# Optimization experiments

Measured on AMD Instinct MI355X. Metric: run time of the kernel, lower is better.

## Reference

```python
import jax, jax.numpy as jnp
import numpy as np

N, E, D, C, H1 = 50000, 800000, 128, 8, 2


def setup_inputs() -> dict:
    key = jax.random.key(0)
    ks = jax.random.split(key, 14)
    s = lambda k, sh: (jax.random.normal(k, sh, jnp.float32) * 0.05)
    return {
        "x": jax.random.normal(ks[0], (N, D), jnp.float32),
        "edge_index": jax.random.randint(ks[1], (2, E), 0, N, dtype=jnp.int32),
        # conv1: GATConv(D, D, heads=2, concat=True)
        "W1": s(ks[2], (D, H1 * D)),
        "att1_src": s(ks[3], (H1, D)),
        "att1_dst": s(ks[4], (H1, D)),
        "b1": s(ks[5], (H1 * D,)),
        # conv2: GATConv(2D, D, heads=1, concat=False)
        "W2": s(ks[6], (H1 * D, D)),
        "att2_src": s(ks[7], (1, D)),
        "att2_dst": s(ks[8], (1, D)),
        "b2": s(ks[9], (D,)),
        # MLP head
        "Wm1": s(ks[10], (D, D)),
        "bm1": s(ks[11], (D,)),
        "Wm2": s(ks[12], (D, C)),
        "bm2": s(ks[13], (C,)),
    }


def gat_conv(x, src, dst, W, a_src, a_dst, b, heads, out_ch, concat):
    """PyG GATConv (eval mode): self-loops added by caller, softmax over
    edges grouped by destination node, negative_slope=0.2."""
    n = x.shape[0]
    h = (x @ W).reshape(n, heads, out_ch)              # [N,H,F]
    alpha_src = jnp.einsum('nhf,hf->nh', h, a_src)     # [N,H]
    alpha_dst = jnp.einsum('nhf,hf->nh', h, a_dst)     # [N,H]
    e = jax.nn.leaky_relu(alpha_src[src] + alpha_dst[dst], 0.2)  # [E,H]
    e_max = jax.ops.segment_max(e, dst, num_segments=n)
    ex = jnp.exp(e - e_max[dst])
    denom = jax.ops.segment_sum(ex, dst, num_segments=n)
    alpha = ex / jnp.maximum(denom[dst], 1e-16)        # [E,H]
    out = jax.ops.segment_sum(h[src] * alpha[:, :, None], dst, num_segments=n)
    out = out.reshape(n, heads * out_ch) if concat else out.mean(axis=1)
    return out + b


def reference(x, edge_index, W1, att1_src, att1_dst, b1,
              W2, att2_src, att2_dst, b2, Wm1, bm1, Wm2, bm2):
    n = x.shape[0]
    loop = jnp.arange(n, dtype=edge_index.dtype)
    src = jnp.concatenate([edge_index[0], loop])  # add_self_loops=True
    dst = jnp.concatenate([edge_index[1], loop])
    h = jax.nn.elu(gat_conv(x, src, dst, W1, att1_src, att1_dst, b1, H1, D, True))
    h = jax.nn.elu(gat_conv(h, src, dst, W2, att2_src, att2_dst, b2, 1, D, False))
    h = jax.nn.relu(h @ Wm1 + bm1)
    return jax.nn.relu(h @ Wm2 + bm2)
```

## Files before the change

kernel.cpp:

```cpp
#include <hip/hip_runtime.h>
#include <hip/hip_bf16.h>


__device__ __forceinline__ float lrelu(float x){ return x > 0.f ? x : 0.2f*x; }
__device__ __forceinline__ float elu_f(float x){ return x > 0.f ? x : __expf(x) - 1.f; }
__device__ __forceinline__ unsigned short f2bf(float f){
  __hip_bfloat16 h = __float2bfloat16(f);
  return *reinterpret_cast<unsigned short*>(&h);
}
__device__ __forceinline__ float bflo(unsigned int u){ return __uint_as_float(u << 16); }
__device__ __forceinline__ float bfhi(unsigned int u){ return __uint_as_float(u & 0xffff0000u); }
__device__ __forceinline__ unsigned int packbf(float a, float b){
  return (unsigned int)f2bf(a) | ((unsigned int)f2bf(b) << 16);
}

typedef __attribute__((ext_vector_type(8))) short bf16x8;
typedef __attribute__((ext_vector_type(4))) float f32x4;

__global__ void prep_kernel(const float* __restrict__ W1, unsigned short* __restrict__ BT1a,
                            unsigned short* __restrict__ BT1b,
                            const float* __restrict__ W2, unsigned short* __restrict__ BT2,
                            const float* __restrict__ Wm1, unsigned short* __restrict__ BT3,
                            const float* __restrict__ a1s, const float* __restrict__ a1d,
                            float* __restrict__ va, int* __restrict__ bcount,
                            int* __restrict__ gcur, int NB){
  int idx = blockIdx.x*256 + threadIdx.x;
  const int S1 = 128*256, S2 = 128*256, S3 = 128*128;
  if (idx < S1){
    int k = idx >> 8, c = idx & 255;
    unsigned short v = f2bf(W1[idx]);
    if (c < 128) BT1a[c*128 + k] = v;
    else         BT1b[(c-128)*128 + k] = v;
  } else if (idx < S1 + S2){
    int j = idx - S1;
    int k = j >> 7, n = j & 127;
    BT2[n*256 + k] = f2bf(W2[j]);
  } else if (idx < S1 + S2 + S3){
    int j = idx - S1 - S2;
    int k = j >> 7, n = j & 127;
    BT3[n*128 + k] = f2bf(Wm1[j]);
  } else if (idx < S1 + S2 + S3 + 512){
    int j = idx - S1 - S2 - S3;
    int v = j >> 7, k = j & 127;
    const float* avec = (v < 2) ? a1s : a1d;
    int head = v & 1;
    const float4* wrow = (const float4*)(W1 + (size_t)k*256 + head*128);
    const float4* arow = (const float4*)(avec + head*128);
    float s = 0.f;
    #pragma unroll 8
    for (int f = 0; f < 32; ++f){
      float4 w = wrow[f], a = arow[f];
      s += w.x*a.x + w.y*a.y + w.z*a.z + w.w*a.w;
    }
    va[j] = s;
  } else if (idx < S1 + S2 + S3 + 512 + 2048){
    int z = idx - (S1 + S2 + S3 + 512);
    if (z < 1024){ if (z < NB) bcount[z] = 0; }
    else { z -= 1024; if (z < NB) gcur[z] = 0; }
  }
}

__global__ __launch_bounds__(256) void f2bf_hist_kernel(
    const float* __restrict__ x, unsigned short* __restrict__ xb, int N,
    const float* __restrict__ va, float* __restrict__ as1, float* __restrict__ ad1,
    const int* __restrict__ dst, int E, int* __restrict__ bcount, int NB, int nbConv)
{
  __shared__ int h[1024];
  if ((int)blockIdx.x < nbConv){
    int i = blockIdx.x*256 + threadIdx.x;
    int total = N*32;
    float4 v = make_float4(0.f,0.f,0.f,0.f);
    if (i < total){
      v = ((const float4*)x)[i];
      ushort4 u; u.x=f2bf(v.x); u.y=f2bf(v.y); u.z=f2bf(v.z); u.w=f2bf(v.w);
      ((ushort4*)xb)[i] = u;
    }
    int c = (i & 31) << 2;
    float4 vs0 = *(const float4*)(va + c);
    float4 vs1 = *(const float4*)(va + 128 + c);
    float4 vd0 = *(const float4*)(va + 256 + c);
    float4 vd1 = *(const float4*)(va + 384 + c);
    float s0 = v.x*vs0.x + v.y*vs0.y + v.z*vs0.z + v.w*vs0.w;
    float s1 = v.x*vs1.x + v.y*vs1.y + v.z*vs1.z + v.w*vs1.w;
    float d0 = v.x*vd0.x + v.y*vd0.y + v.z*vd0.z + v.w*vd0.w;
    float d1 = v.x*vd1.x + v.y*vd1.y + v.z*vd1.z + v.w*vd1.w;
    #pragma unroll
    for (int m = 1; m <= 16; m <<= 1){
      s0 += __shfl_xor(s0, m); s1 += __shfl_xor(s1, m);
      d0 += __shfl_xor(d0, m); d1 += __shfl_xor(d1, m);
    }
    if ((i & 31) == 0 && i < total){
      int n = i >> 5;
      *(float2*)(as1 + 2*n) = make_float2(s0, s1);
      *(float2*)(ad1 + 2*n) = make_float2(d0, d1);
    }
  } else {
    for (int i = threadIdx.x; i < NB; i += 256) h[i] = 0;
    __syncthreads();
    int b0 = blockIdx.x - nbConv;
    for (int e = b0*256 + threadIdx.x; e < E; e += 64*256)
      atomicAdd(&h[dst[e] >> 6], 1);
    __syncthreads();
    for (int i = threadIdx.x; i < NB; i += 256)
      if (h[i]) atomicAdd(&bcount[i], h[i]);
  }
}

__global__ __launch_bounds__(256) void bscatter_kernel(
    const int* __restrict__ src, const int* __restrict__ dst, int E,
    const int* __restrict__ bcount, int* __restrict__ boff,
    int* __restrict__ gcur, unsigned int* __restrict__ pairs, int NB)
{
  __shared__ int h[1024];
  __shared__ int runbase[1024];
  __shared__ int sc[1024];
  const int t = threadIdx.x;
  const int e0 = blockIdx.x * 4096;

  for (int i = t; i < 1024; i += 256) sc[i] = (i < NB) ? bcount[i] : 0;
  for (int i = t; i < NB; i += 256) h[i] = 0;
  __syncthreads();
  for (int d = 1; d < 1024; d <<= 1){
    int v0 = (t       >= d) ? sc[t       - d] : 0;
    int v1 = (t + 256 >= d) ? sc[t + 256 - d] : 0;
    int v2 = (t + 512 >= d) ? sc[t + 512 - d] : 0;
    int v3 = (t + 768 >= d) ? sc[t + 768 - d] : 0;
    __syncthreads();
    sc[t] += v0; sc[t+256] += v1; sc[t+512] += v2; sc[t+768] += v3;
    __syncthreads();
  }
  if (blockIdx.x == 0){
    for (int i = t; i <= NB; i += 256) boff[i] = i ? sc[i-1] : 0;
  }

  int myb[16]; unsigned int myw[16];
  #pragma unroll
  for (int q = 0; q < 16; ++q){
    int e = e0 + q*256 + t;
    int b = -1; unsigned int w = 0;
    if (e < E){
      int d = dst[e];
      b = d >> 6;
      w = ((unsigned int)(d & 63) << 26) | (unsigned int)src[e];
      atomicAdd(&h[b], 1);
    }
    myb[q] = b; myw[q] = w;
  }
  __syncthreads();
  for (int i = t; i < NB; i += 256)
    runbase[i] = h[i] ? atomicAdd(&gcur[i], h[i]) : 0;
  __syncthreads();
  for (int i = t; i < NB; i += 256) h[i] = 0;
  __syncthreads();
  #pragma unroll
  for (int q = 0; q < 16; ++q){
    if (myb[q] >= 0){
      int off = atomicAdd(&h[myb[q]], 1);
      int base = myb[q] ? sc[myb[q]-1] : 0;
      pairs[(size_t)base + runbase[myb[q]] + off] = myw[q];
    }
  }
}

__global__ __launch_bounds__(256) void bbuild_kernel(
    const unsigned int* __restrict__ pairs, const int* __restrict__ boff,
    int* __restrict__ rowptr, int* __restrict__ csr, int N)
{
  __shared__ int deg[64], offs[64], cur[64];
  const int b = blockIdx.x;
  const int t = threadIdx.x;
  const int n0 = b << 6;
  const int nNodes = min(64, N - n0);
  const int p0 = boff[b], p1 = boff[b+1];
  const int base = p0 + n0;
  if (t < 64) deg[t] = (t < nNodes) ? 1 : 0;
  __syncthreads();
  for (int i = p0 + t; i < p1; i += 256)
    atomicAdd(&deg[pairs[i] >> 26], 1);
  __syncthreads();
  if (t < 64){
    int x = deg[t];
    #pragma unroll
    for (int d = 1; d < 64; d <<= 1){
      int y = __shfl_up(x, d);
      if (t >= d) x += y;
    }
    offs[t] = x - deg[t];
    cur[t] = 1;
    if (t < nNodes){
      rowptr[n0 + t + 1] = base + x;
      csr[base + x - deg[t]] = n0 + t;
    }
    if (b == 0 && t == 0) rowptr[0] = 0;
  }
  __syncthreads();
  for (int i = p0 + t; i < p1; i += 256){
    unsigned int w = pairs[i];
    int dl = w >> 26;
    int s  = (int)(w & 0x03ffffffu);
    int off = atomicAdd(&cur[dl], 1);
    csr[base + offs[dl] + off] = s;
  }
}

__device__ __forceinline__ void gemm_core(
    const unsigned short* __restrict__ A, int lda,
    const unsigned short* __restrict__ BT, int M, int K, int r0,
    unsigned short* a_s, unsigned short* b_s, f32x4 (&acc)[4][4])
{
  const int tid  = threadIdx.x;
  const int lane = tid & 63, wv = tid >> 6;
  const int mh = (wv & 1)*64, nh = (wv >> 1)*64;
  const int l15 = lane & 15, quad = lane >> 4;
  const int srow = tid >> 3, skc = tid & 7;

  #pragma unroll
  for (int i = 0; i < 4; ++i)
    #pragma unroll
    for (int j = 0; j < 4; ++j)
      #pragma unroll
      for (int r = 0; r < 4; ++r) acc[i][j][r] = 0.f;

  for (int k0 = 0; k0 < K; k0 += 64){
    #pragma unroll
    for (int it = 0; it < 4; ++it){
      int row = it*32 + srow;
      int grow = r0 + row;
      uint4 v = make_uint4(0u,0u,0u,0u);
      if (grow < M) v = *(const uint4*)(A + (size_t)grow*lda + k0 + skc*8);
      *(uint4*)(&a_s[row*72 + skc*8]) = v;
    }
    #pragma unroll
    for (int it = 0; it < 4; ++it){
      int row = it*32 + srow;
      uint4 v = *(const uint4*)(BT + (size_t)row*K + k0 + skc*8);
      *(uint4*)(&b_s[row*72 + skc*8]) = v;
    }
    __syncthreads();
    #pragma unroll
    for (int ks = 0; ks < 64; ks += 32){
      bf16x8 af[4], bfr[4];
      #pragma unroll
      for (int i = 0; i < 4; ++i)
        af[i] = *(const bf16x8*)(&a_s[(mh + i*16 + l15)*72 + ks + quad*8]);
      #pragma unroll
      for (int j = 0; j < 4; ++j)
        bfr[j] = *(const bf16x8*)(&b_s[(nh + j*16 + l15)*72 + ks + quad*8]);
      #pragma unroll
      for (int i = 0; i < 4; ++i)
        #pragma unroll
        for (int j = 0; j < 4; ++j)
          acc[i][j] = __builtin_amdgcn_mfma_f32_16x16x32_bf16(bfr[j], af[i], acc[i][j], 0, 0, 0);
    }
    __syncthreads();
  }
}

__global__ __launch_bounds__(256) void gemm_conv1_kernel(
    const unsigned short* __restrict__ xa, const unsigned short* __restrict__ BT1a,
    const unsigned short* __restrict__ BT1b, unsigned short* __restrict__ out1b,
    int M, const float* __restrict__ b1)
{
  __shared__ unsigned short a_s[128*72];
  __shared__ unsigned short b_s[128*72];
  const int hx = blockIdx.x;
  const unsigned short* A  = xa + hx*128;
  const unsigned short* BT = hx ? BT1b : BT1a;
  unsigned short* C = out1b + hx*128;
  const float* bias = b1 + hx*128;
  const int r0 = blockIdx.y*128;
  f32x4 acc[4][4];
  gemm_core(A, 256, BT, M, 128, r0, a_s, b_s, acc);

  const int lane = threadIdx.x & 63, wv = threadIdx.x >> 6;
  const int mh = (wv & 1)*64, nh = (wv >> 1)*64;
  const int l15 = lane & 15, quad = lane >> 4;
  #pragma unroll
  for (int i = 0; i < 4; ++i){
    int m = r0 + mh + i*16 + l15;
    if (m < M){
      #pragma unroll
      for (int j = 0; j < 4; ++j){
        int n = nh + j*16 + quad*4;
        float4 bb = *(const float4*)(bias + n);
        ushort4 u;
        u.x = f2bf(elu_f(acc[i][j][0] + bb.x));
        u.y = f2bf(elu_f(acc[i][j][1] + bb.y));
        u.z = f2bf(elu_f(acc[i][j][2] + bb.z));
        u.w = f2bf(elu_f(acc[i][j][3] + bb.w));
        *(ushort4*)(C + (size_t)m*256 + n) = u;
      }
    }
  }
}

__global__ __launch_bounds__(256) void gemm_conv2_kernel(
    const unsigned short* __restrict__ out1b, const unsigned short* __restrict__ BT2,
    unsigned short* __restrict__ h2b, int M,
    const float* __restrict__ a2s, const float* __restrict__ a2d,
    float* __restrict__ as2, float* __restrict__ ad2)
{
  __shared__ unsigned short a_s[128*72];
  __shared__ unsigned short b_s[128*72];
  __shared__ float part_s[128][2];
  __shared__ float part_d[128][2];
  const int r0 = blockIdx.y*128;
  f32x4 acc[4][4];
  gemm_core(out1b, 256, BT2, M, 256, r0, a_s, b_s, acc);

  const int tid = threadIdx.x;
  const int lane = tid & 63, wv = tid >> 6;
  const int mh = (wv & 1)*64, nh = (wv >> 1)*64;
  const int l15 = lane & 15, quad = lane >> 4;
  #pragma unroll
  for (int i = 0; i < 4; ++i){
    int m = r0 + mh + i*16 + l15;
    float ps = 0.f, pd = 0.f;
    #pragma unroll
    for (int j = 0; j < 4; ++j){
      int n = nh + j*16 + quad*4;
      float4 wsv = *(const float4*)(a2s + n);
      float4 wdv = *(const float4*)(a2d + n);
      float v0 = acc[i][j][0], v1 = acc[i][j][1], v2 = acc[i][j][2], v3 = acc[i][j][3];
      ps += v0*wsv.x + v1*wsv.y + v2*wsv.z + v3*wsv.w;
      pd += v0*wdv.x + v1*wdv.y + v2*wdv.z + v3*wdv.w;
      if (m < M){
        ushort4 u;
        u.x = f2bf(v0); u.y = f2bf(v1); u.z = f2bf(v2); u.w = f2bf(v3);
        *(ushort4*)(h2b + (size_t)m*128 + n) = u;
      }
    }
    ps += __shfl_xor(ps, 16); ps += __shfl_xor(ps, 32);
    pd += __shfl_xor(pd, 16); pd += __shfl_xor(pd, 32);
    if (quad == 0){
      part_s[mh + i*16 + l15][wv >> 1] = ps;
      part_d[mh + i*16 + l15][wv >> 1] = pd;
    }
  }
  __syncthreads();
  if (tid < 128){
    int gm = r0 + tid;
    if (gm < M){
      as2[gm] = part_s[tid][0] + part_s[tid][1];
      ad2[gm] = part_d[tid][0] + part_d[tid][1];
    }
  }
}

__global__ __launch_bounds__(256) void gemm_mlp_kernel(
    const unsigned short* __restrict__ gb, const unsigned short* __restrict__ BT3,
    int M, const float* __restrict__ bm1, const float* __restrict__ Wm2,
    const float* __restrict__ bm2, float* __restrict__ out)
{
  __shared__ unsigned short a_s[128*72];
  __shared__ unsigned short b_s[128*72];
  __shared__ float wm2_s[128*8];
  __shared__ float part[128][2][8];
  const int tid = threadIdx.x;
  {
    int i4 = tid*4;
    *(float4*)(&wm2_s[i4]) = *(const float4*)(Wm2 + i4);
  }
  const int r0 = blockIdx.y*128;
  f32x4 acc[4][4];
  gemm_core(gb, 128, BT3, M, 128, r0, a_s, b_s, acc);

  const int lane = tid & 63, wv = tid >> 6;
  const int mh = (wv & 1)*64, nh = (wv >> 1)*64;
  const int l15 = lane & 15, quad = lane >> 4;
  #pragma unroll
  for (int i = 0; i < 4; ++i){
    float po[8];
    #pragma unroll
    for (int o = 0; o < 8; ++o) po[o] = 0.f;
    #pragma unroll
    for (int j = 0; j < 4; ++j){
      int n = nh + j*16 + quad*4;
      float4 bb = *(const float4*)(bm1 + n);
      #pragma unroll
      for (int r = 0; r < 4; ++r){
        float hcol = fmaxf(acc[i][j][r] + ((const float*)&bb)[r], 0.f);
        const float* wr = &wm2_s[(n + r)*8];
        #pragma unroll
        for (int o = 0; o < 8; ++o) po[o] += hcol*wr[o];
      }
    }
    #pragma unroll
    for (int o = 0; o < 8; ++o){
      po[o] += __shfl_xor(po[o], 16);
      po[o] += __shfl_xor(po[o], 32);
    }
    if (quad == 0){
      #pragma unroll
      for (int o = 0; o < 8; ++o) part[mh + i*16 + l15][wv >> 1][o] = po[o];
    }
  }
  __syncthreads();
  if (tid < 128){
    int gm = r0 + tid;
    if (gm < M){
      float4 o0, o1;
      o0.x = fmaxf(part[tid][0][0] + part[tid][1][0] + bm2[0], 0.f);
      o0.y = fmaxf(part[tid][0][1] + part[tid][1][1] + bm2[1], 0.f);
      o0.z = fmaxf(part[tid][0][2] + part[tid][1][2] + bm2[2], 0.f);
      o0.w = fmaxf(part[tid][0][3] + part[tid][1][3] + bm2[3], 0.f);
      o1.x = fmaxf(part[tid][0][4] + part[tid][1][4] + bm2[4], 0.f);
      o1.y = fmaxf(part[tid][0][5] + part[tid][1][5] + bm2[5], 0.f);
      o1.z = fmaxf(part[tid][0][6] + part[tid][1][6] + bm2[6], 0.f);
      o1.w = fmaxf(part[tid][0][7] + part[tid][1][7] + bm2[7], 0.f);
      *(float4*)(out + (size_t)gm*8)     = o0;
      *(float4*)(out + (size_t)gm*8 + 4) = o1;
    }
  }
}

#define AGG1_FMA(u, a0v, a1v) do{ \
    float f0 = bflo(u.x), f1 = bfhi(u.x), f2v = bflo(u.y), f3 = bfhi(u.y); \
    float f4 = bflo(u.z), f5 = bfhi(u.z), f6 = bflo(u.w), f7 = bfhi(u.w); \
    acc0[0] += a0v*f0; acc0[1] += a0v*f1; acc0[2] += a0v*f2v; acc0[3] += a0v*f3; \
    acc0[4] += a0v*f4; acc0[5] += a0v*f5; acc0[6] += a0v*f6;  acc0[7] += a0v*f7; \
    acc1[0] += a1v*f0; acc1[1] += a1v*f1; acc1[2] += a1v*f2v; acc1[3] += a1v*f3; \
    acc1[4] += a1v*f4; acc1[5] += a1v*f5; acc1[6] += a1v*f6;  acc1[7] += a1v*f7; \
  }while(0)

#define AGG2_FMA(u, av) do{ \
    acc[0] += av*bflo(u.x); acc[1] += av*bfhi(u.x); \
    acc[2] += av*bflo(u.y); acc[3] += av*bfhi(u.y); \
    acc[4] += av*bflo(u.z); acc[5] += av*bfhi(u.z); \
    acc[6] += av*bflo(u.w); acc[7] += av*bfhi(u.w); \
  }while(0)

__global__ __launch_bounds__(256) void agg1x_kernel(
    const unsigned short* __restrict__ xb, const float* __restrict__ as_,
    const float* __restrict__ ad_, const int* __restrict__ rowptr, const int* __restrict__ csr,
    unsigned short* __restrict__ xa, int N)
{
  const int wv = threadIdx.x >> 6, lane = threadIdx.x & 63;
  const int ql = lane & 15;
  const int n = blockIdx.x*16 + wv*4 + (lane >> 4);
  const bool valid = n < N;
  int start = 0, end = 0;
  float2 adv = make_float2(0.f, 0.f);
  if (valid){ start = rowptr[n]; end = rowptr[n+1]; adv = *(const float2*)(ad_ + 2*n); }

  int jl = start + ql;
  bool have = valid && (jl < end);
  int s_l = 0;
  float p0 = 0.f, p1 = 0.f;
  if (have){
    s_l = csr[jl];
    float2 av = *(const float2*)(as_ + 2*s_l);
    p0 = __expf(lrelu(av.x + adv.x));
    p1 = __expf(lrelu(av.y + adv.y));
  }
  float l0 = p0, l1 = p1;
  for (int j = jl + 16; j < end; j += 16){
    int s = csr[j];
    float2 av = *(const float2*)(as_ + 2*s);
    l0 += __expf(lrelu(av.x + adv.x));
    l1 += __expf(lrelu(av.y + adv.y));
  }
  #pragma unroll
  for (int msk = 1; msk <= 8; msk <<= 1){
    l0 += __shfl_xor(l0, msk);
    l1 += __shfl_xor(l1, msk);
  }
  float inv0 = 1.f / fmaxf(l0, 1e-16f);
  float inv1 = 1.f / fmaxf(l1, 1e-16f);
  float a0_l = p0 * inv0;
  float a1_l = p1 * inv1;

  float acc0[8], acc1[8];
  #pragma unroll
  for (int i = 0; i < 8; ++i){ acc0[i] = 0.f; acc1[i] = 0.f; }
  const int c = ql << 3;
  const unsigned short* hp = xb + c;

  #pragma unroll
  for (int half = 0; half < 2; ++half){
    uint4 u[8]; float b0[8], b1[8];
    #pragma unroll
    for (int t = 0; t < 8; ++t){
      int tt = half*8 + t;
      int sA = __shfl(s_l, tt, 16);
      b0[t] = __shfl(a0_l, tt, 16);
      b1[t] = __shfl(a1_l, tt, 16);
      u[t] = *(const uint4*)(hp + (sA << 7));
    }
    #pragma unroll
    for (int t = 0; t < 8; ++t) AGG1_FMA(u[t], b0[t], b1[t]);
  }
  for (int jb = start + 16; jb < end; jb += 16){
    int jl2 = jb + ql;
    int s2 = 0; float a0_2 = 0.f, a1_2 = 0.f;
    if (jl2 < end){
      s2 = csr[jl2];
      float2 av = *(const float2*)(as_ + 2*s2);
      a0_2 = __expf(lrelu(av.x + adv.x)) * inv0;
      a1_2 = __expf(lrelu(av.y + adv.y)) * inv1;
    }
    int cnt2 = min(16, end - jb);
    for (int t2 = 0; t2 < cnt2; t2 += 2){
      int   sA  = __shfl(s2, t2, 16),   sB  = __shfl(s2, t2+1, 16);
      float a0A = __shfl(a0_2, t2, 16), a0B = __shfl(a0_2, t2+1, 16);
      float a1A = __shfl(a1_2, t2, 16), a1B = __shfl(a1_2, t2+1, 16);
      uint4 uA = *(const uint4*)(hp + (sA << 7));
      uint4 uB = *(const uint4*)(hp + (sB << 7));
      AGG1_FMA(uA, a0A, a1A);
      AGG1_FMA(uB, a0B, a1B);
    }
  }

  if (valid){
    uint4 u0, u1;
    u0.x = packbf(acc0[0], acc0[1]); u0.y = packbf(acc0[2], acc0[3]);
    u0.z = packbf(acc0[4], acc0[5]); u0.w = packbf(acc0[6], acc0[7]);
    u1.x = packbf(acc1[0], acc1[1]); u1.y = packbf(acc1[2], acc1[3]);
    u1.z = packbf(acc1[4], acc1[5]); u1.w = packbf(acc1[6], acc1[7]);
    *(uint4*)(xa + (size_t)n*256 + c)       = u0;
    *(uint4*)(xa + (size_t)n*256 + 128 + c) = u1;
  }
}

__global__ __launch_bounds__(256) void agg2_kernel(
    const unsigned short* __restrict__ h2b, const float* __restrict__ as_,
    const float* __restrict__ ad_, const int* __restrict__ rowptr, const int* __restrict__ csr,
    const float* __restrict__ b2, unsigned short* __restrict__ outb, int N)
{
  const int wv = threadIdx.x >> 6, lane = threadIdx.x & 63;
  const int ql = lane & 15;
  const int n = blockIdx.x*16 + wv*4 + (lane >> 4);
  const bool valid = n < N;
  int start = 0, end = 0;
  float adn = 0.f;
  if (valid){ start = rowptr[n]; end = rowptr[n+1]; adn = ad_[n]; }

  int jl = start + ql;
  bool have = valid && (jl < end);
  int s_l = 0;
  float p_l = 0.f;
  if (have){
    s_l = csr[jl];
    p_l = __expf(lrelu(as_[s_l] + adn));
  }
  float l = p_l;
  for (int j = jl + 16; j < end; j += 16)
    l += __expf(lrelu(as_[csr[j]] + adn));
  #pragma unroll
  for (int msk = 1; msk <= 8; msk <<= 1) l += __shfl_xor(l, msk);
  float inv = 1.f / fmaxf(l, 1e-16f);
  float a_l = p_l * inv;

  float acc[8];
  #pragma unroll
  for (int i = 0; i < 8; ++i) acc[i] = 0.f;
  const int c = ql << 3;
  const unsigned short* hp = h2b + c;

  #pragma unroll
  for (int half = 0; half < 2; ++half){
    uint4 u[8]; float av[8];
    #pragma unroll
    for (int t = 0; t < 8; ++t){
      int tt = half*8 + t;
      int sA = __shfl(s_l, tt, 16);
      av[t] = __shfl(a_l, tt, 16);
      u[t] = *(const uint4*)(hp + (sA << 7));
    }
    #pragma unroll
    for (int t = 0; t < 8; ++t) AGG2_FMA(u[t], av[t]);
  }
  for (int jb = start + 16; jb < end; jb += 16){
    int jl2 = jb + ql;
    int s2 = 0; float a2 = 0.f;
    if (jl2 < end){
      s2 = csr[jl2];
      a2 = __expf(lrelu(as_[s2] + adn)) * inv;
    }
    int cnt2 = min(16, end - jb);
    for (int t2 = 0; t2 < cnt2; t2 += 2){
      int   sA = __shfl(s2, t2, 16),  sB = __shfl(s2, t2+1, 16);
      float aA = __shfl(a2, t2, 16),  aB = __shfl(a2, t2+1, 16);
      uint4 uA = *(const uint4*)(hp + (sA << 7));
      uint4 uB = *(const uint4*)(hp + (sB << 7));
      AGG2_FMA(uA, aA);
      AGG2_FMA(uB, aB);
    }
  }

  if (valid){
    float4 bb0 = *(const float4*)(b2 + c);
    float4 bb1 = *(const float4*)(b2 + c + 4);
    float o[8];
    o[0]=elu_f(acc[0]+bb0.x); o[1]=elu_f(acc[1]+bb0.y);
    o[2]=elu_f(acc[2]+bb0.z); o[3]=elu_f(acc[3]+bb0.w);
    o[4]=elu_f(acc[4]+bb1.x); o[5]=elu_f(acc[5]+bb1.y);
    o[6]=elu_f(acc[6]+bb1.z); o[7]=elu_f(acc[7]+bb1.w);
    uint4 up;
    up.x = packbf(o[0], o[1]); up.y = packbf(o[2], o[3]);
    up.z = packbf(o[4], o[5]); up.w = packbf(o[6], o[7]);
    *(uint4*)(outb + (size_t)n*128 + c) = up;
  }
}

extern "C" void kernel_launch(void* const* d_in, const int* in_sizes, int n_in,
                              void* d_out, int out_size, void* d_ws, size_t ws_size,
                              hipStream_t stream)
{
  (void)n_in; (void)out_size; (void)ws_size;
  const float* x   = (const float*)d_in[0];
  const int*   ei  = (const int*)d_in[1];
  const float* W1  = (const float*)d_in[2];
  const float* a1s = (const float*)d_in[3];
  const float* a1d = (const float*)d_in[4];
  const float* b1  = (const float*)d_in[5];
  const float* W2  = (const float*)d_in[6];
  const float* a2s = (const float*)d_in[7];
  const float* a2d = (const float*)d_in[8];
  const float* b2  = (const float*)d_in[9];
  const float* Wm1 = (const float*)d_in[10];
  const float* bm1 = (const float*)d_in[11];
  const float* Wm2 = (const float*)d_in[12];
  const float* bm2 = (const float*)d_in[13];
  float* out = (float*)d_out;

  const int N = in_sizes[0] / 128;
  const int E = in_sizes[1] / 2;
  const int NB = (N + 63) >> 6;
  const int* srcp = ei;
  const int* dstp = ei + E;

  char* ws = (char*)d_ws;
  unsigned short* xb    = (unsigned short*)ws;
  unsigned short* xa    = (unsigned short*)(ws + (size_t)N*256);
  unsigned short* out1b = (unsigned short*)(ws + (size_t)N*768);
  unsigned short* h2b   = (unsigned short*)(ws + (size_t)N*1280);
  char* tail = ws + (size_t)N*1536;
  unsigned short* BT1a = (unsigned short*)tail;
  unsigned short* BT1b = BT1a + 128*128;
  unsigned short* BT2  = BT1b + 128*128;
  unsigned short* BT3  = BT2 + 128*256;
  float* va   = (float*)(BT3 + 128*128);
  float* as1  = va + 512;
  float* ad1  = as1 + (size_t)2*N;
  float* as2  = ad1 + (size_t)2*N;
  float* ad2  = as2 + N;
  int* bcount = (int*)(ad2 + N);
  int* boff   = bcount + 1024;
  int* gcur   = boff + 1032;
  int* rowptr = gcur + 1024;
  int* csr    = rowptr + N + 1;
  unsigned int* pairs = (unsigned int*)(csr + E + N);

  unsigned short* gb = xb;

  const int nbConv = (N*32 + 255)/256;
  const int prepTotal = 128*256 + 128*256 + 128*128 + 512 + 2048;

  prep_kernel<<<(prepTotal + 255)/256, 256, 0, stream>>>(
      W1, BT1a, BT1b, W2, BT2, Wm1, BT3, a1s, a1d, va, bcount, gcur, NB);
  f2bf_hist_kernel<<<nbConv + 64, 256, 0, stream>>>(x, xb, N, va, as1, ad1,
                                                    dstp, E, bcount, NB, nbConv);
  bscatter_kernel<<<(E + 4095)/4096, 256, 0, stream>>>(srcp, dstp, E, bcount, boff, gcur, pairs, NB);
  bbuild_kernel<<<NB, 256, 0, stream>>>(pairs, boff, rowptr, csr, N);

  const int nb16 = (N + 15) / 16;
  const int gy   = (N + 127) / 128;

  agg1x_kernel<<<nb16, 256, 0, stream>>>(xb, as1, ad1, rowptr, csr, xa, N);
  gemm_conv1_kernel<<<dim3(2, gy), 256, 0, stream>>>(xa, BT1a, BT1b, out1b, N, b1);
  gemm_conv2_kernel<<<dim3(1, gy), 256, 0, stream>>>(out1b, BT2, h2b, N, a2s, a2d, as2, ad2);
  agg2_kernel<<<nb16, 256, 0, stream>>>(h2b, as2, ad2, rowptr, csr, b2, gb, N);
  gemm_mlp_kernel<<<dim3(1, gy), 256, 0, stream>>>(gb, BT3, N, bm1, Wm2, bm2, out);
}
```

Before: 263.1 us.

## Fuse conv1 and conv2 GEMMs, keeping the intermediate tile in shared memory

Merges the two back-to-back GEMM kernels into one 512-thread kernel over 64-row tiles. The ELU-activated conv1 output for a tile is held in LDS and fed straight into the conv2 GEMM. This removes the out1b global buffer round trip (write plus re-read of N×256 bf16) and one launch. The cost is smaller tiles, so weight tiles are reloaded more often, plus higher LDS use per block, which may limit occupancy.

```diff
diff --git a/kernel.cpp b/kernel.cpp
--- a/kernel.cpp
+++ b/kernel.cpp
@@ -256,72 +256,129 @@
   }
 }
 
-__global__ __launch_bounds__(256) void gemm_conv1_kernel(
-    const unsigned short* __restrict__ xa, const unsigned short* __restrict__ BT1a,
-    const unsigned short* __restrict__ BT1b, unsigned short* __restrict__ out1b,
-    int M, const float* __restrict__ b1)
-{
-  __shared__ unsigned short a_s[128*72];
+__global__ __launch_bounds__(512, 2) void gemm_conv12_kernel(
+    const unsigned short* __restrict__ xa,
+    const unsigned short* __restrict__ BT1a, const unsigned short* __restrict__ BT1b,
+    const float* __restrict__ b1, const unsigned short* __restrict__ BT2,
+    unsigned short* __restrict__ h2b, int M,
+    const float* __restrict__ a2s, const float* __restrict__ a2d,
+    float* __restrict__ as2, float* __restrict__ ad2)
+{
+  __shared__ unsigned short t_s[64*264];
+  __shared__ unsigned short a_s[64*72];
   __shared__ unsigned short b_s[128*72];
-  const int hx = blockIdx.x;
-  const unsigned short* A  = xa + hx*128;
-  const unsigned short* BT = hx ? BT1b : BT1a;
-  unsigned short* C = out1b + hx*128;
-  const float* bias = b1 + hx*128;
-  const int r0 = blockIdx.y*128;
-  f32x4 acc[4][4];
-  gemm_core(A, 256, BT, M, 128, r0, a_s, b_s, acc);
-
-  const int lane = threadIdx.x & 63, wv = threadIdx.x >> 6;
-  const int mh = (wv & 1)*64, nh = (wv >> 1)*64;
+  __shared__ float part_s[64][4];
+  __shared__ float part_d[64][4];
+
+  const int tid = threadIdx.x;
+  const int lane = tid & 63, wv = tid >> 6;
   const int l15 = lane & 15, quad = lane >> 4;
-  #pragma unroll
-  for (int i = 0; i < 4; ++i){
-    int m = r0 + mh + i*16 + l15;
-    if (m < M){
-      #pragma unroll
-      for (int j = 0; j < 4; ++j){
-        int n = nh + j*16 + quad*4;
-        float4 bb = *(const float4*)(bias + n);
+  const int r0 = blockIdx.x*64;
+  const int mh = (wv & 1)*32;
+  const int nhp = (wv >> 1)*32;
+
+  const int arow = tid >> 3, askc = tid & 7;
+  const int brow = tid >> 2, bc2 = (tid & 3)*2;
+  #pragma unroll
+  for (int h = 0; h < 2; ++h){
+    const unsigned short* BT = h ? BT1b : BT1a;
+    f32x4 acc[2][2];
+    #pragma unroll
+    for (int i = 0; i < 2; ++i)
+      #pragma unroll
+      for (int j = 0; j < 2; ++j)
+        #pragma unroll
+        for (int r = 0; r < 4; ++r) acc[i][j][r] = 0.f;
+
+    for (int k0 = 0; k0 < 128; k0 += 64){
+      {
+        int grow = r0 + arow;
+        uint4 v = make_uint4(0u,0u,0u,0u);
+        if (grow < M) v = *(const uint4*)(xa + (size_t)grow*256 + h*128 + k0 + askc*8);
+        *(uint4*)(&a_s[arow*72 + askc*8]) = v;
+      }
+      {
+        *(uint4*)(&b_s[brow*72 + bc2*8])     = *(const uint4*)(BT + (size_t)brow*128 + k0 + bc2*8);
+        *(uint4*)(&b_s[brow*72 + (bc2+1)*8]) = *(const uint4*)(BT + (size_t)brow*128 + k0 + (bc2+1)*8);
+      }
+      __syncthreads();
+      #pragma unroll
+      for (int ks = 0; ks < 64; ks += 32){
+        bf16x8 af[2], bfr[2];
+        #pragma unroll
+        for (int i = 0; i < 2; ++i)
+          af[i] = *(const bf16x8*)(&a_s[(mh + i*16 + l15)*72 + ks + quad*8]);
+        #pragma unroll
+        for (int j = 0; j < 2; ++j)
+          bfr[j] = *(const bf16x8*)(&b_s[(nhp + j*16 + l15)*72 + ks + quad*8]);
+        #pragma unroll
+        for (int i = 0; i < 2; ++i)
+          #pragma unroll
+          for (int j = 0; j < 2; ++j)
+            acc[i][j] = __builtin_amdgcn_mfma_f32_16x16x32_bf16(bfr[j], af[i], acc[i][j], 0, 0, 0);
+      }
+      __syncthreads();
+    }
+    #pragma unroll
+    for (int i = 0; i < 2; ++i){
+      int row = mh + i*16 + l15;
+      #pragma unroll
+      for (int j = 0; j < 2; ++j){
+        int n = nhp + j*16 + quad*4;
+        float4 bb = *(const float4*)(b1 + h*128 + n);
         ushort4 u;
         u.x = f2bf(elu_f(acc[i][j][0] + bb.x));
         u.y = f2bf(elu_f(acc[i][j][1] + bb.y));
         u.z = f2bf(elu_f(acc[i][j][2] + bb.z));
         u.w = f2bf(elu_f(acc[i][j][3] + bb.w));
-        *(ushort4*)(C + (size_t)m*256 + n) = u;
+        *(ushort4*)(&t_s[row*264 + h*128 + n]) = u;
       }
     }
   }
-}
-
-__global__ __launch_bounds__(256) void gemm_conv2_kernel(
-    const unsigned short* __restrict__ out1b, const unsigned short* __restrict__ BT2,
-    unsigned short* __restrict__ h2b, int M,
-    const float* __restrict__ a2s, const float* __restrict__ a2d,
-    float* __restrict__ as2, float* __restrict__ ad2)
-{
-  __shared__ unsigned short a_s[128*72];
-  __shared__ unsigned short b_s[128*72];
-  __shared__ float part_s[128][2];
-  __shared__ float part_d[128][2];
-  const int r0 = blockIdx.y*128;
-  f32x4 acc[4][4];
-  gemm_core(out1b, 256, BT2, M, 256, r0, a_s, b_s, acc);
-
-  const int tid = threadIdx.x;
-  const int lane = tid & 63, wv = tid >> 6;
-  const int mh = (wv & 1)*64, nh = (wv >> 1)*64;
-  const int l15 = lane & 15, quad = lane >> 4;
-  #pragma unroll
-  for (int i = 0; i < 4; ++i){
+  __syncthreads();
+
+  f32x4 acc2[2][2];
+  #pragma unroll
+  for (int i = 0; i < 2; ++i)
+    #pragma unroll
+    for (int j = 0; j < 2; ++j)
+      #pragma unroll
+      for (int r = 0; r < 4; ++r) acc2[i][j][r] = 0.f;
+
+  for (int k0 = 0; k0 < 256; k0 += 64){
+    {
+      *(uint4*)(&b_s[brow*72 + bc2*8])     = *(const uint4*)(BT2 + (size_t)brow*256 + k0 + bc2*8);
+      *(uint4*)(&b_s[brow*72 + (bc2+1)*8]) = *(const uint4*)(BT2 + (size_t)brow*256 + k0 + (bc2+1)*8);
+    }
+    __syncthreads();
+    #pragma unroll
+    for (int ks = 0; ks < 64; ks += 32){
+      bf16x8 af[2], bfr[2];
+      #pragma unroll
+      for (int i = 0; i < 2; ++i)
+        af[i] = *(const bf16x8*)(&t_s[(mh + i*16 + l15)*264 + k0 + ks + quad*8]);
+      #pragma unroll
+      for (int j = 0; j < 2; ++j)
+        bfr[j] = *(const bf16x8*)(&b_s[(nhp + j*16 + l15)*72 + ks + quad*8]);
+      #pragma unroll
+      for (int i = 0; i < 2; ++i)
+        #pragma unroll
+        for (int j = 0; j < 2; ++j)
+          acc2[i][j] = __builtin_amdgcn_mfma_f32_16x16x32_bf16(bfr[j], af[i], acc2[i][j], 0, 0, 0);
+    }
+    __syncthreads();
+  }
+
+  #pragma unroll
+  for (int i = 0; i < 2; ++i){
     int m = r0 + mh + i*16 + l15;
     float ps = 0.f, pd = 0.f;
     #pragma unroll
-    for (int j = 0; j < 4; ++j){
-      int n = nh + j*16 + quad*4;
+    for (int j = 0; j < 2; ++j){
+      int n = nhp + j*16 + quad*4;
       float4 wsv = *(const float4*)(a2s + n);
       float4 wdv = *(const float4*)(a2d + n);
-      float v0 = acc[i][j][0], v1 = acc[i][j][1], v2 = acc[i][j][2], v3 = acc[i][j][3];
+      float v0 = acc2[i][j][0], v1 = acc2[i][j][1], v2 = acc2[i][j][2], v3 = acc2[i][j][3];
       ps += v0*wsv.x + v1*wsv.y + v2*wsv.z + v3*wsv.w;
       pd += v0*wdv.x + v1*wdv.y + v2*wdv.z + v3*wdv.w;
       if (m < M){
@@ -338,11 +395,11 @@
     }
   }
   __syncthreads();
-  if (tid < 128){
+  if (tid < 64){
     int gm = r0 + tid;
     if (gm < M){
-      as2[gm] = part_s[tid][0] + part_s[tid][1];
-      ad2[gm] = part_d[tid][0] + part_d[tid][1];
+      as2[gm] = part_s[tid][0] + part_s[tid][1] + part_s[tid][2] + part_s[tid][3];
+      ad2[gm] = part_d[tid][0] + part_d[tid][1] + part_d[tid][2] + part_d[tid][3];
     }
   }
 }
@@ -633,9 +690,8 @@
   char* ws = (char*)d_ws;
   unsigned short* xb    = (unsigned short*)ws;
   unsigned short* xa    = (unsigned short*)(ws + (size_t)N*256);
-  unsigned short* out1b = (unsigned short*)(ws + (size_t)N*768);
-  unsigned short* h2b   = (unsigned short*)(ws + (size_t)N*1280);
-  char* tail = ws + (size_t)N*1536;
+  unsigned short* h2b   = (unsigned short*)(ws + (size_t)N*768);
+  char* tail = ws + (size_t)N*1024;
   unsigned short* BT1a = (unsigned short*)tail;
   unsigned short* BT1b = BT1a + 128*128;
   unsigned short* BT2  = BT1b + 128*128;
@@ -665,11 +721,12 @@
   bbuild_kernel<<<NB, 256, 0, stream>>>(pairs, boff, rowptr, csr, N);
 
   const int nb16 = (N + 15) / 16;
+  const int g64  = (N + 63) / 64;
   const int gy   = (N + 127) / 128;
 
   agg1x_kernel<<<nb16, 256, 0, stream>>>(xb, as1, ad1, rowptr, csr, xa, N);
-  gemm_conv1_kernel<<<dim3(2, gy), 256, 0, stream>>>(xa, BT1a, BT1b, out1b, N, b1);
-  gemm_conv2_kernel<<<dim3(1, gy), 256, 0, stream>>>(out1b, BT2, h2b, N, a2s, a2d, as2, ad2);
+  gemm_conv12_kernel<<<g64, 512, 0, stream>>>(xa, BT1a, BT1b, b1, BT2,
+                                              h2b, N, a2s, a2d, as2, ad2);
   agg2_kernel<<<nb16, 256, 0, stream>>>(h2b, as2, ad2, rowptr, csr, b2, gb, N);
   gemm_mlp_kernel<<<dim3(1, gy), 256, 0, stream>>>(gb, BT3, N, bm1, Wm2, bm2, out);
 }
```

After: 250.9 us (median of 2 runs). 4.6% less time.
